# Kernel optimization log

Hardware: AMD Instinct MI355X
Metric: run time of the kernel (lower is better)

Reference implementation:

```python
import jax, jax.numpy as jnp
import numpy as np

N_NODES = 100000
N_EDGES = 1600000
IN_F, HID, N_CLS = 512, 64, 32


def gcn_conv(x, edge_index, W, b, num_nodes):
    """PyG GCNConv: h = D^{-1/2} (A+I) D^{-1/2} (x W) + b."""
    loop = jnp.arange(num_nodes)
    src = jnp.concatenate([edge_index[0], loop])  # [E+N]
    dst = jnp.concatenate([edge_index[1], loop])
    # degree of target nodes (incl. self-loops)
    deg = jax.ops.segment_sum(jnp.ones_like(dst, dtype=x.dtype), dst,
                              num_segments=num_nodes)
    dinv = jnp.where(deg > 0, jax.lax.rsqrt(deg), 0.0)
    norm = dinv[src] * dinv[dst]  # [E+N]
    h = x @ W  # dense transform first (matches PyG: small out dim)
    msgs = h[src] * norm[:, None]  # edge-wise gather + scale
    out = jax.ops.segment_sum(msgs, dst, num_segments=num_nodes)  # scatter-add
    return out + b


def setup_inputs() -> dict:
    key = jax.random.key(0)
    k1, k2, k3, k4, k5, k6 = jax.random.split(key, 6)
    x = jax.random.normal(k1, (N_NODES, IN_F), dtype=jnp.float32)
    edge_index = jax.random.randint(k2, (2, N_EDGES), 0, N_NODES, dtype=jnp.int64)
    # Glorot-style init for the two GCNConv weights + biases
    W1 = jax.random.normal(k3, (IN_F, HID), dtype=jnp.float32) / np.sqrt(IN_F)
    b1 = jnp.zeros((HID,), dtype=jnp.float32)
    W2 = jax.random.normal(k4, (HID, N_CLS), dtype=jnp.float32) / np.sqrt(HID)
    b2 = jnp.zeros((N_CLS,), dtype=jnp.float32)
    return {"x": x, "edge_index": edge_index, "W1": W1, "b1": b1,
            "W2": W2, "b2": b2}


def reference(x, edge_index, W1, b1, W2, b2):
    num_nodes = x.shape[0]
    h = jax.nn.relu(gcn_conv(x, edge_index, W1, b1, num_nodes))
    z = gcn_conv(h, edge_index, W2, b2, num_nodes)
    return (h, z)
```

## Files before the change

### kernel.cpp

```cpp
#include <hip/hip_runtime.h>

#define N_NODES 100000
#define N_EDGES 1600000
#define IN_F 512
#define HID 64
#define N_CLS 32
#define NBKT2 391
#define EBLK 8192
#define NBLKA ((N_EDGES + EBLK - 1) / EBLK)

typedef __attribute__((ext_vector_type(8))) short short8;
typedef __attribute__((ext_vector_type(4))) float f32x4;

__device__ __forceinline__ unsigned short f2bf(float f) {
  unsigned int u = __float_as_uint(f);
  u += 0x7FFFu + ((u >> 16) & 1u);
  return (unsigned short)(u >> 16);
}
__device__ __forceinline__ float bf2f(unsigned int s) {
  return __uint_as_float(s << 16);
}

__global__ __launch_bounds__(256) void coarse_hist_k(const int* __restrict__ ei,
                                                     int* __restrict__ bcnt) {
  __shared__ int lh[NBKT2];
  int tid = threadIdx.x;
  for (int b = tid; b < NBKT2; b += 256) lh[b] = 0;
  __syncthreads();
  int e0 = blockIdx.x * EBLK;
  int e1 = min(e0 + EBLK, N_EDGES);
  for (int e = e0 + tid; e < e1; e += 256)
    atomicAdd(&lh[ei[N_EDGES + e] >> 8], 1);
  __syncthreads();
  for (int b = tid; b < NBKT2; b += 256) {
    int c = lh[b];
    if (c) atomicAdd(&bcnt[b], c);
  }
}

__global__ __launch_bounds__(512) void coarse_scan_k(const int* __restrict__ bcnt,
                                                     int* __restrict__ bbase,
                                                     int* __restrict__ bcur) {
  __shared__ int sc[512];
  int tid = threadIdx.x;
  int v = (tid < NBKT2) ? bcnt[tid] : 0;
  sc[tid] = v;
  __syncthreads();
  for (int off = 1; off < 512; off <<= 1) {
    int t = (tid >= off) ? sc[tid - off] : 0;
    __syncthreads();
    sc[tid] += t;
    __syncthreads();
  }
  int incl = sc[tid];
  int excl = incl - v;
  if (tid < NBKT2) { bbase[tid] = excl; bcur[tid] = excl; }
  if (tid == NBKT2 - 1) bbase[NBKT2] = incl;
}

__global__ __launch_bounds__(256) void passA_k(const int* __restrict__ ei,
                                               int* __restrict__ bcur,
                                               unsigned* __restrict__ tmp) {
  __shared__ int lhist[NBKT2];
  __shared__ int gcur[NBKT2];
  int tid = threadIdx.x;
  int e0 = blockIdx.x * EBLK;
  int e1 = min(e0 + EBLK, N_EDGES);
  for (int b = tid; b < NBKT2; b += 256) lhist[b] = 0;
  __syncthreads();
  for (int e = e0 + tid; e < e1; e += 256) {
    int d = ei[N_EDGES + e];
    atomicAdd(&lhist[d >> 8], 1);
  }
  __syncthreads();
  for (int b = tid; b < NBKT2; b += 256) {
    int c = lhist[b];
    gcur[b] = c ? atomicAdd(&bcur[b], c) : 0;
  }
  __syncthreads();
  for (int e = e0 + tid; e < e1; e += 256) {
    int s = ei[e], d = ei[N_EDGES + e];
    int p = atomicAdd(&gcur[d >> 8], 1);
    tmp[p] = ((unsigned)s << 8) | (unsigned)(d & 255);
  }
}

__global__ __launch_bounds__(256) void passB_k(const unsigned* __restrict__ tmp,
                                               const int* __restrict__ bbase,
                                               int* __restrict__ rowptr,
                                               float* __restrict__ dinv,
                                               int* __restrict__ srcs) {
  __shared__ int sc[256];
  __shared__ int cur[256];
  int b = blockIdx.x, tid = threadIdx.x;
  int n0 = b << 8;
  int n1 = min(n0 + 256, N_NODES);
  int base = bbase[b], end = bbase[b + 1];
  sc[tid] = 0;
  __syncthreads();
  for (int i = base + tid; i < end; i += 256)
    atomicAdd(&sc[tmp[i] & 255u], 1);
  __syncthreads();
  int myc = sc[tid];
  for (int off = 1; off < 256; off <<= 1) {
    int t = (tid >= off) ? sc[tid - off] : 0;
    __syncthreads();
    sc[tid] += t;
    __syncthreads();
  }
  int incl = sc[tid];
  int excl = incl - myc;
  if (n0 + tid < n1) {
    rowptr[n0 + tid + 1] = base + incl;
    dinv[n0 + tid] = rsqrtf((float)(myc + 1));
  }
  if (b == 0 && tid == 0) rowptr[0] = 0;
  cur[tid] = base + excl;
  __syncthreads();
  for (int i = base + tid; i < end; i += 256) {
    unsigned v = tmp[i];
    int p = atomicAdd(&cur[v & 255u], 1);
    srcs[p] = (int)(v >> 8);
  }
}

__global__ __launch_bounds__(256) void w1t_k(const float* __restrict__ W1,
                                             unsigned short* __restrict__ W1t) {
  int i = blockIdx.x * 256 + threadIdx.x;
  if (i < IN_F * HID) {
    int n = i >> 9, k = i & 511;
    W1t[i] = f2bf(W1[(size_t)k * HID + n]);
  }
}

__global__ __launch_bounds__(256) void gemm1_mfma_k(const float* __restrict__ x,
                                                    const unsigned short* __restrict__ W1t,
                                                    const float* __restrict__ dinv,
                                                    unsigned short* __restrict__ h0s) {
  __shared__ __align__(16) char As[64 * 128];
  __shared__ __align__(16) char Ws[64 * 128];
  int tid = threadIdx.x;
  int wave = tid >> 6, lane = tid & 63;
  int row0 = blockIdx.x * 64;
  f32x4 acc[4] = {{0.f,0.f,0.f,0.f},{0.f,0.f,0.f,0.f},{0.f,0.f,0.f,0.f},{0.f,0.f,0.f,0.f}};

  int l15 = lane & 15, lhi = lane >> 4;
  int rA = (wave << 4) + l15;

  for (int k0 = 0; k0 < IN_F; k0 += 64) {
    #pragma unroll
    for (int i = 0; i < 4; ++i) {
      int f = tid + i * 256;
      int r = f >> 4, c4 = (f & 15) << 2;
      float4 v = make_float4(0.f, 0.f, 0.f, 0.f);
      int gr = row0 + r;
      if (gr < N_NODES) v = *(const float4*)(x + (size_t)gr * IN_F + k0 + c4);
      ushort4 u;
      u.x = f2bf(v.x); u.y = f2bf(v.y); u.z = f2bf(v.z); u.w = f2bf(v.w);
      int byte = r * 128 + (c4 << 1);
      byte ^= (r & 7) << 4;
      *(ushort4*)(As + byte) = u;
    }
    #pragma unroll
    for (int i = 0; i < 2; ++i) {
      int f = tid + i * 256;
      int n = f >> 3, k8 = (f & 7) << 3;
      uint4 v = *(const uint4*)(W1t + (size_t)n * IN_F + k0 + k8);
      int byte = n * 128 + (k8 << 1);
      byte ^= (n & 7) << 4;
      *(uint4*)(Ws + byte) = v;
    }
    __syncthreads();
    #pragma unroll
    for (int ks = 0; ks < 64; ks += 32) {
      int kk = ks + (lhi << 3);
      int ba = rA * 128 + (kk << 1); ba ^= (rA & 7) << 4;
      short8 a = *(const short8*)(As + ba);
      #pragma unroll
      for (int j = 0; j < 4; ++j) {
        int nB = (j << 4) + l15;
        int bb = nB * 128 + (kk << 1); bb ^= (nB & 7) << 4;
        short8 bv = *(const short8*)(Ws + bb);
        acc[j] = __builtin_amdgcn_mfma_f32_16x16x32_bf16(a, bv, acc[j], 0, 0, 0);
      }
    }
    __syncthreads();
  }
  int rbase = row0 + (wave << 4) + (lhi << 2);
  #pragma unroll
  for (int r = 0; r < 4; ++r) {
    int gr = rbase + r;
    if (gr < N_NODES) {
      float dn = dinv[gr];
      #pragma unroll
      for (int j = 0; j < 4; ++j)
        h0s[(size_t)gr * HID + (j << 4) + l15] = f2bf(dn * acc[j][r]);
    }
  }
}

__global__ __launch_bounds__(256) void agg1_k(const uint4* __restrict__ h0q,
                                              const int* __restrict__ rowptr,
                                              const int* __restrict__ srcs,
                                              const float* __restrict__ dinv,
                                              const float* __restrict__ b1,
                                              float* __restrict__ out) {
  int idx = blockIdx.x * 256 + threadIdx.x;
  int node = idx >> 6;
  if (node >= N_NODES) return;
  int lane = threadIdx.x & 63;
  int fl = lane & 7, g = lane >> 3;
  int p0 = rowptr[node], p1 = rowptr[node + 1];
  int c = p1 - p0;
  int ps = p0 + ((c * g) >> 3);
  int pe = p0 + ((c * (g + 1)) >> 3);
  float a[8] = {0.f,0.f,0.f,0.f,0.f,0.f,0.f,0.f};
  if (g == 0) {
    uint4 u = h0q[(size_t)node * 8 + fl];
    a[0] = bf2f(u.x & 0xffffu); a[1] = bf2f(u.x >> 16);
    a[2] = bf2f(u.y & 0xffffu); a[3] = bf2f(u.y >> 16);
    a[4] = bf2f(u.z & 0xffffu); a[5] = bf2f(u.z >> 16);
    a[6] = bf2f(u.w & 0xffffu); a[7] = bf2f(u.w >> 16);
  }
  int p = ps;
  for (; p + 2 <= pe; p += 2) {
    int s0 = srcs[p], s1 = srcs[p + 1];
    uint4 u0 = h0q[(size_t)s0 * 8 + fl];
    uint4 u1 = h0q[(size_t)s1 * 8 + fl];
    a[0] += bf2f(u0.x & 0xffffu) + bf2f(u1.x & 0xffffu);
    a[1] += bf2f(u0.x >> 16)     + bf2f(u1.x >> 16);
    a[2] += bf2f(u0.y & 0xffffu) + bf2f(u1.y & 0xffffu);
    a[3] += bf2f(u0.y >> 16)     + bf2f(u1.y >> 16);
    a[4] += bf2f(u0.z & 0xffffu) + bf2f(u1.z & 0xffffu);
    a[5] += bf2f(u0.z >> 16)     + bf2f(u1.z >> 16);
    a[6] += bf2f(u0.w & 0xffffu) + bf2f(u1.w & 0xffffu);
    a[7] += bf2f(u0.w >> 16)     + bf2f(u1.w >> 16);
  }
  if (p < pe) {
    uint4 u = h0q[(size_t)srcs[p] * 8 + fl];
    a[0] += bf2f(u.x & 0xffffu); a[1] += bf2f(u.x >> 16);
    a[2] += bf2f(u.y & 0xffffu); a[3] += bf2f(u.y >> 16);
    a[4] += bf2f(u.z & 0xffffu); a[5] += bf2f(u.z >> 16);
    a[6] += bf2f(u.w & 0xffffu); a[7] += bf2f(u.w >> 16);
  }
  #pragma unroll
  for (int off = 8; off < 64; off <<= 1) {
    #pragma unroll
    for (int i = 0; i < 8; ++i) a[i] += __shfl_xor(a[i], off);
  }
  if (g == 0) {
    float dn = dinv[node];
    float4 bA = *(const float4*)(b1 + fl * 8);
    float4 bB = *(const float4*)(b1 + fl * 8 + 4);
    float4 s0, s1;
    s0.x = fmaxf(dn * a[0] + bA.x, 0.f); s0.y = fmaxf(dn * a[1] + bA.y, 0.f);
    s0.z = fmaxf(dn * a[2] + bA.z, 0.f); s0.w = fmaxf(dn * a[3] + bA.w, 0.f);
    s1.x = fmaxf(dn * a[4] + bB.x, 0.f); s1.y = fmaxf(dn * a[5] + bB.y, 0.f);
    s1.z = fmaxf(dn * a[6] + bB.z, 0.f); s1.w = fmaxf(dn * a[7] + bB.w, 0.f);
    *(float4*)(out + (size_t)node * HID + fl * 8) = s0;
    *(float4*)(out + (size_t)node * HID + fl * 8 + 4) = s1;
  }
}

__global__ __launch_bounds__(256) void gemm2_k(const float* __restrict__ h,
                                               const float* __restrict__ W2,
                                               const float* __restrict__ dinv,
                                               unsigned short* __restrict__ h2b) {
  __shared__ float w2s[HID * N_CLS];
  __shared__ float hs[32][HID];
  int tid = threadIdx.x;
  for (int i = tid; i < HID * N_CLS; i += 256) w2s[i] = W2[i];
  int node0 = blockIdx.x * 32;
  for (int i = tid; i < 32 * HID / 4; i += 256) {
    int r = i >> 4, c4 = (i & 15) << 2;
    int g = node0 + r;
    float4 v = make_float4(0.f, 0.f, 0.f, 0.f);
    if (g < N_NODES) v = *(const float4*)(h + (size_t)g * HID + c4);
    *(float4*)&hs[r][c4] = v;
  }
  __syncthreads();
  int cls = tid & 31, nl = tid >> 5;
  float acc[4] = {0.f, 0.f, 0.f, 0.f};
  #pragma unroll
  for (int k = 0; k < HID; ++k) {
    float w = w2s[k * N_CLS + cls];
    #pragma unroll
    for (int j = 0; j < 4; ++j) acc[j] += hs[nl * 4 + j][k] * w;
  }
  #pragma unroll
  for (int j = 0; j < 4; ++j) {
    int g = node0 + nl * 4 + j;
    if (g < N_NODES) h2b[(size_t)g * N_CLS + cls] = f2bf(dinv[g] * acc[j]);
  }
}

__global__ __launch_bounds__(256) void agg2_k(const uint2* __restrict__ h2u,
                                              const int* __restrict__ rowptr,
                                              const int* __restrict__ srcs,
                                              const float* __restrict__ dinv,
                                              const float* __restrict__ b2,
                                              float* __restrict__ out) {
  int idx = blockIdx.x * 256 + threadIdx.x;
  int node = idx >> 6;
  if (node >= N_NODES) return;
  int lane = threadIdx.x & 63;
  int fl = lane & 7, g = lane >> 3;
  int p0 = rowptr[node], p1 = rowptr[node + 1];
  int c = p1 - p0;
  int ps = p0 + ((c * g) >> 3);
  int pe = p0 + ((c * (g + 1)) >> 3);
  float a0 = 0.f, a1 = 0.f, a2 = 0.f, a3 = 0.f;
  if (g == 0) {
    uint2 u = h2u[(size_t)node * 8 + fl];
    a0 = bf2f(u.x & 0xffffu); a1 = bf2f(u.x >> 16);
    a2 = bf2f(u.y & 0xffffu); a3 = bf2f(u.y >> 16);
  }
  int p = ps;
  for (; p + 2 <= pe; p += 2) {
    int s0 = srcs[p], s1 = srcs[p + 1];
    uint2 u0 = h2u[(size_t)s0 * 8 + fl];
    uint2 u1 = h2u[(size_t)s1 * 8 + fl];
    a0 += bf2f(u0.x & 0xffffu) + bf2f(u1.x & 0xffffu);
    a1 += bf2f(u0.x >> 16)     + bf2f(u1.x >> 16);
    a2 += bf2f(u0.y & 0xffffu) + bf2f(u1.y & 0xffffu);
    a3 += bf2f(u0.y >> 16)     + bf2f(u1.y >> 16);
  }
  if (p < pe) {
    uint2 u = h2u[(size_t)srcs[p] * 8 + fl];
    a0 += bf2f(u.x & 0xffffu); a1 += bf2f(u.x >> 16);
    a2 += bf2f(u.y & 0xffffu); a3 += bf2f(u.y >> 16);
  }
  #pragma unroll
  for (int off = 8; off < 64; off <<= 1) {
    a0 += __shfl_xor(a0, off); a1 += __shfl_xor(a1, off);
    a2 += __shfl_xor(a2, off); a3 += __shfl_xor(a3, off);
  }
  if (g == 0) {
    float dn = dinv[node];
    float4 bv = *(const float4*)(b2 + fl * 4);
    float4 st;
    st.x = dn * a0 + bv.x; st.y = dn * a1 + bv.y;
    st.z = dn * a2 + bv.z; st.w = dn * a3 + bv.w;
    *(float4*)(out + (size_t)node * N_CLS + fl * 4) = st;
  }
}

extern "C" void kernel_launch(void* const* d_in, const int* in_sizes, int n_in,
                              void* d_out, int out_size, void* d_ws, size_t ws_size,
                              hipStream_t stream) {
  const float* x  = (const float*)d_in[0];
  const int*   ei = (const int*)d_in[1];
  const float* W1 = (const float*)d_in[2];
  const float* b1 = (const float*)d_in[3];
  const float* W2 = (const float*)d_in[4];
  const float* b2 = (const float*)d_in[5];
  float* out_h = (float*)d_out;
  float* out_z = out_h + (size_t)N_NODES * HID;

  char* ws = (char*)d_ws;
  int* bcnt           = (int*)(ws + 0);
  int* bbase          = (int*)(ws + (4 << 10));
  int* bcur           = (int*)(ws + (8 << 10));
  int* rowptr         = (int*)(ws + (16 << 10));
  float* dinv         = (float*)(ws + (528 << 10));
  unsigned short* W1t = (unsigned short*)(ws + (944 << 10));
  unsigned* tmp       = (unsigned*)(ws + (1024 << 10));
  int* srcs           = (int*)(ws + (8ull << 20));
  unsigned short* h0s = (unsigned short*)(ws + (15ull << 20));
  unsigned short* h2b = (unsigned short*)(ws + (28ull << 20));

  hipMemsetAsync(bcnt, 0, NBKT2 * sizeof(int), stream);
  w1t_k<<<(IN_F * HID + 255) / 256, 256, 0, stream>>>(W1, W1t);
  coarse_hist_k<<<NBLKA, 256, 0, stream>>>(ei, bcnt);
  coarse_scan_k<<<1, 512, 0, stream>>>(bcnt, bbase, bcur);
  passA_k<<<NBLKA, 256, 0, stream>>>(ei, bcur, tmp);
  passB_k<<<NBKT2, 256, 0, stream>>>(tmp, bbase, rowptr, dinv, srcs);
  gemm1_mfma_k<<<(N_NODES + 63) / 64, 256, 0, stream>>>(x, W1t, dinv, h0s);
  agg1_k<<<(N_NODES * 64) / 256, 256, 0, stream>>>((const uint4*)h0s, rowptr, srcs, dinv, b1, out_h);
  gemm2_k<<<(N_NODES + 31) / 32, 256, 0, stream>>>(out_h, W2, dinv, h2b);
  agg2_k<<<(N_NODES * 64) / 256, 256, 0, stream>>>((const uint2*)h2b, rowptr, srcs, dinv, b2, out_z);
}
```

Measured before the change: 232.8 us.

## Split features into 16-wide slabs and aggregate each slab in separate passes

The GEMM outputs are now written as slab-major arrays of 16 bf16 features per node (3.2 MB per slab), and the aggregation runs once per slab: four passes for layer 1 and two for layer 2. A single generic kernel replaces both aggregation kernels. The aim is a gather working set small enough to stay in L2/MALL, so random neighbour reads hit cache instead of HBM. In exchange the edge list and rowptr are re-read on every pass, more kernels are launched, and each gather fetches only 4 bytes per lane.

```diff
diff --git a/kernel.cpp b/kernel.cpp
--- a/kernel.cpp
+++ b/kernel.cpp
@@ -136,7 +136,7 @@
 __global__ __launch_bounds__(256) void gemm1_mfma_k(const float* __restrict__ x,
                                                     const unsigned short* __restrict__ W1t,
                                                     const float* __restrict__ dinv,
-                                                    unsigned short* __restrict__ h0s) {
+                                                    unsigned short* __restrict__ h0q) {
   __shared__ __align__(16) char As[64 * 128];
   __shared__ __align__(16) char Ws[64 * 128];
   int tid = threadIdx.x;
@@ -194,78 +194,65 @@
       float dn = dinv[gr];
       #pragma unroll
       for (int j = 0; j < 4; ++j)
-        h0s[(size_t)gr * HID + (j << 4) + l15] = f2bf(dn * acc[j][r]);
+        h0q[((size_t)j * N_NODES + gr) * 16 + l15] = f2bf(dn * acc[j][r]);
     }
   }
 }
 
-__global__ __launch_bounds__(256) void agg1_k(const uint4* __restrict__ h0q,
+__global__ __launch_bounds__(256) void aggq_k(const unsigned* __restrict__ hq,
                                               const int* __restrict__ rowptr,
                                               const int* __restrict__ srcs,
                                               const float* __restrict__ dinv,
-                                              const float* __restrict__ b1,
-                                              float* __restrict__ out) {
+                                              const float* __restrict__ bias,
+                                              float* __restrict__ out,
+                                              int ostride, int do_relu) {
   int idx = blockIdx.x * 256 + threadIdx.x;
   int node = idx >> 6;
   if (node >= N_NODES) return;
   int lane = threadIdx.x & 63;
-  int fl = lane & 7, g = lane >> 3;
+  int ln = lane & 7, g = lane >> 3;
   int p0 = rowptr[node], p1 = rowptr[node + 1];
   int c = p1 - p0;
   int ps = p0 + ((c * g) >> 3);
   int pe = p0 + ((c * (g + 1)) >> 3);
-  float a[8] = {0.f,0.f,0.f,0.f,0.f,0.f,0.f,0.f};
+  float a0 = 0.f, a1 = 0.f;
   if (g == 0) {
-    uint4 u = h0q[(size_t)node * 8 + fl];
-    a[0] = bf2f(u.x & 0xffffu); a[1] = bf2f(u.x >> 16);
-    a[2] = bf2f(u.y & 0xffffu); a[3] = bf2f(u.y >> 16);
-    a[4] = bf2f(u.z & 0xffffu); a[5] = bf2f(u.z >> 16);
-    a[6] = bf2f(u.w & 0xffffu); a[7] = bf2f(u.w >> 16);
+    unsigned u = hq[(size_t)node * 8 + ln];
+    a0 = bf2f(u & 0xffffu); a1 = bf2f(u >> 16);
   }
   int p = ps;
-  for (; p + 2 <= pe; p += 2) {
-    int s0 = srcs[p], s1 = srcs[p + 1];
-    uint4 u0 = h0q[(size_t)s0 * 8 + fl];
-    uint4 u1 = h0q[(size_t)s1 * 8 + fl];
-    a[0] += bf2f(u0.x & 0xffffu) + bf2f(u1.x & 0xffffu);
-    a[1] += bf2f(u0.x >> 16)     + bf2f(u1.x >> 16);
-    a[2] += bf2f(u0.y & 0xffffu) + bf2f(u1.y & 0xffffu);
-    a[3] += bf2f(u0.y >> 16)     + bf2f(u1.y >> 16);
-    a[4] += bf2f(u0.z & 0xffffu) + bf2f(u1.z & 0xffffu);
-    a[5] += bf2f(u0.z >> 16)     + bf2f(u1.z >> 16);
-    a[6] += bf2f(u0.w & 0xffffu) + bf2f(u1.w & 0xffffu);
-    a[7] += bf2f(u0.w >> 16)     + bf2f(u1.w >> 16);
-  }
-  if (p < pe) {
-    uint4 u = h0q[(size_t)srcs[p] * 8 + fl];
-    a[0] += bf2f(u.x & 0xffffu); a[1] += bf2f(u.x >> 16);
-    a[2] += bf2f(u.y & 0xffffu); a[3] += bf2f(u.y >> 16);
-    a[4] += bf2f(u.z & 0xffffu); a[5] += bf2f(u.z >> 16);
-    a[6] += bf2f(u.w & 0xffffu); a[7] += bf2f(u.w >> 16);
+  for (; p + 4 <= pe; p += 4) {
+    int s0 = srcs[p], s1 = srcs[p + 1], s2 = srcs[p + 2], s3 = srcs[p + 3];
+    unsigned u0 = hq[(size_t)s0 * 8 + ln];
+    unsigned u1 = hq[(size_t)s1 * 8 + ln];
+    unsigned u2 = hq[(size_t)s2 * 8 + ln];
+    unsigned u3 = hq[(size_t)s3 * 8 + ln];
+    a0 += (bf2f(u0 & 0xffffu) + bf2f(u1 & 0xffffu)) + (bf2f(u2 & 0xffffu) + bf2f(u3 & 0xffffu));
+    a1 += (bf2f(u0 >> 16) + bf2f(u1 >> 16)) + (bf2f(u2 >> 16) + bf2f(u3 >> 16));
+  }
+  for (; p < pe; ++p) {
+    unsigned u = hq[(size_t)srcs[p] * 8 + ln];
+    a0 += bf2f(u & 0xffffu); a1 += bf2f(u >> 16);
   }
   #pragma unroll
   for (int off = 8; off < 64; off <<= 1) {
-    #pragma unroll
-    for (int i = 0; i < 8; ++i) a[i] += __shfl_xor(a[i], off);
+    a0 += __shfl_xor(a0, off);
+    a1 += __shfl_xor(a1, off);
   }
   if (g == 0) {
     float dn = dinv[node];
-    float4 bA = *(const float4*)(b1 + fl * 8);
-    float4 bB = *(const float4*)(b1 + fl * 8 + 4);
-    float4 s0, s1;
-    s0.x = fmaxf(dn * a[0] + bA.x, 0.f); s0.y = fmaxf(dn * a[1] + bA.y, 0.f);
-    s0.z = fmaxf(dn * a[2] + bA.z, 0.f); s0.w = fmaxf(dn * a[3] + bA.w, 0.f);
-    s1.x = fmaxf(dn * a[4] + bB.x, 0.f); s1.y = fmaxf(dn * a[5] + bB.y, 0.f);
-    s1.z = fmaxf(dn * a[6] + bB.z, 0.f); s1.w = fmaxf(dn * a[7] + bB.w, 0.f);
-    *(float4*)(out + (size_t)node * HID + fl * 8) = s0;
-    *(float4*)(out + (size_t)node * HID + fl * 8 + 4) = s1;
+    float2 st;
+    st.x = dn * a0 + bias[ln * 2];
+    st.y = dn * a1 + bias[ln * 2 + 1];
+    if (do_relu) { st.x = fmaxf(st.x, 0.f); st.y = fmaxf(st.y, 0.f); }
+    *(float2*)(out + (size_t)node * ostride + ln * 2) = st;
   }
 }
 
 __global__ __launch_bounds__(256) void gemm2_k(const float* __restrict__ h,
                                                const float* __restrict__ W2,
                                                const float* __restrict__ dinv,
-                                               unsigned short* __restrict__ h2b) {
+                                               unsigned short* __restrict__ h2h) {
   __shared__ float w2s[HID * N_CLS];
   __shared__ float hs[32][HID];
   int tid = threadIdx.x;
@@ -280,6 +267,7 @@
   }
   __syncthreads();
   int cls = tid & 31, nl = tid >> 5;
+  int half = cls >> 4, cl = cls & 15;
   float acc[4] = {0.f, 0.f, 0.f, 0.f};
   #pragma unroll
   for (int k = 0; k < HID; ++k) {
@@ -290,58 +278,7 @@
   #pragma unroll
   for (int j = 0; j < 4; ++j) {
     int g = node0 + nl * 4 + j;
-    if (g < N_NODES) h2b[(size_t)g * N_CLS + cls] = f2bf(dinv[g] * acc[j]);
-  }
-}
-
-__global__ __launch_bounds__(256) void agg2_k(const uint2* __restrict__ h2u,
-                                              const int* __restrict__ rowptr,
-                                              const int* __restrict__ srcs,
-                                              const float* __restrict__ dinv,
-                                              const float* __restrict__ b2,
-                                              float* __restrict__ out) {
-  int idx = blockIdx.x * 256 + threadIdx.x;
-  int node = idx >> 6;
-  if (node >= N_NODES) return;
-  int lane = threadIdx.x & 63;
-  int fl = lane & 7, g = lane >> 3;
-  int p0 = rowptr[node], p1 = rowptr[node + 1];
-  int c = p1 - p0;
-  int ps = p0 + ((c * g) >> 3);
-  int pe = p0 + ((c * (g + 1)) >> 3);
-  float a0 = 0.f, a1 = 0.f, a2 = 0.f, a3 = 0.f;
-  if (g == 0) {
-    uint2 u = h2u[(size_t)node * 8 + fl];
-    a0 = bf2f(u.x & 0xffffu); a1 = bf2f(u.x >> 16);
-    a2 = bf2f(u.y & 0xffffu); a3 = bf2f(u.y >> 16);
-  }
-  int p = ps;
-  for (; p + 2 <= pe; p += 2) {
-    int s0 = srcs[p], s1 = srcs[p + 1];
-    uint2 u0 = h2u[(size_t)s0 * 8 + fl];
-    uint2 u1 = h2u[(size_t)s1 * 8 + fl];
-    a0 += bf2f(u0.x & 0xffffu) + bf2f(u1.x & 0xffffu);
-    a1 += bf2f(u0.x >> 16)     + bf2f(u1.x >> 16);
-    a2 += bf2f(u0.y & 0xffffu) + bf2f(u1.y & 0xffffu);
-    a3 += bf2f(u0.y >> 16)     + bf2f(u1.y >> 16);
-  }
-  if (p < pe) {
-    uint2 u = h2u[(size_t)srcs[p] * 8 + fl];
-    a0 += bf2f(u.x & 0xffffu); a1 += bf2f(u.x >> 16);
-    a2 += bf2f(u.y & 0xffffu); a3 += bf2f(u.y >> 16);
-  }
-  #pragma unroll
-  for (int off = 8; off < 64; off <<= 1) {
-    a0 += __shfl_xor(a0, off); a1 += __shfl_xor(a1, off);
-    a2 += __shfl_xor(a2, off); a3 += __shfl_xor(a3, off);
-  }
-  if (g == 0) {
-    float dn = dinv[node];
-    float4 bv = *(const float4*)(b2 + fl * 4);
-    float4 st;
-    st.x = dn * a0 + bv.x; st.y = dn * a1 + bv.y;
-    st.z = dn * a2 + bv.z; st.w = dn * a3 + bv.w;
-    *(float4*)(out + (size_t)node * N_CLS + fl * 4) = st;
+    if (g < N_NODES) h2h[((size_t)half * N_NODES + g) * 16 + cl] = f2bf(dinv[g] * acc[j]);
   }
 }
 
@@ -366,8 +303,8 @@
   unsigned short* W1t = (unsigned short*)(ws + (944 << 10));
   unsigned* tmp       = (unsigned*)(ws + (1024 << 10));
   int* srcs           = (int*)(ws + (8ull << 20));
-  unsigned short* h0s = (unsigned short*)(ws + (15ull << 20));
-  unsigned short* h2b = (unsigned short*)(ws + (28ull << 20));
+  unsigned short* h0q = (unsigned short*)(ws + (15ull << 20));
+  unsigned short* h2h = (unsigned short*)(ws + (28ull << 20));
 
   hipMemsetAsync(bcnt, 0, NBKT2 * sizeof(int), stream);
   w1t_k<<<(IN_F * HID + 255) / 256, 256, 0, stream>>>(W1, W1t);
@@ -375,8 +312,14 @@
   coarse_scan_k<<<1, 512, 0, stream>>>(bcnt, bbase, bcur);
   passA_k<<<NBLKA, 256, 0, stream>>>(ei, bcur, tmp);
   passB_k<<<NBKT2, 256, 0, stream>>>(tmp, bbase, rowptr, dinv, srcs);
-  gemm1_mfma_k<<<(N_NODES + 63) / 64, 256, 0, stream>>>(x, W1t, dinv, h0s);
-  agg1_k<<<(N_NODES * 64) / 256, 256, 0, stream>>>((const uint4*)h0s, rowptr, srcs, dinv, b1, out_h);
-  gemm2_k<<<(N_NODES + 31) / 32, 256, 0, stream>>>(out_h, W2, dinv, h2b);
-  agg2_k<<<(N_NODES * 64) / 256, 256, 0, stream>>>((const uint2*)h2b, rowptr, srcs, dinv, b2, out_z);
-}
+  gemm1_mfma_k<<<(N_NODES + 63) / 64, 256, 0, stream>>>(x, W1t, dinv, h0q);
+  for (int q = 0; q < 4; ++q)
+    aggq_k<<<(N_NODES * 64) / 256, 256, 0, stream>>>(
+        (const unsigned*)(h0q + (size_t)q * N_NODES * 16), rowptr, srcs, dinv,
+        b1 + q * 16, out_h + q * 16, HID, 1);
+  gemm2_k<<<(N_NODES + 31) / 32, 256, 0, stream>>>(out_h, W2, dinv, h2h);
+  for (int q = 0; q < 2; ++q)
+    aggq_k<<<(N_NODES * 64) / 256, 256, 0, stream>>>(
+        (const unsigned*)(h2h + (size_t)q * N_NODES * 16), rowptr, srcs, dinv,
+        b2 + q * 16, out_z + q * 16, N_CLS, 0);
+}
```

Result: slower. 368.7 us (+58.3%).

## Fuse layer-2 dense transform into agg1 and reuse per-block edge histograms

Applied to the files above, without the earlier changes.

Fuses the second-layer 64x32 matmul into the first aggregation kernel: each wave writes its relu output row to shared memory and immediately computes the scaled bf16 h2 row, removing the gemm2 kernel and its re-read of out_h. coarse_hist now stores per-block bucket counts so passA no longer re-reads destinations and rebuilds its local histogram. The memset is folded into the W1 transpose kernel. In exchange, every agg1 block reloads W2 into shared memory, and the fused kernel adds shared memory and register use, which may lower occupancy.

```diff
diff --git a/kernel.cpp b/kernel.cpp
--- a/kernel.cpp
+++ b/kernel.cpp
@@ -21,8 +21,20 @@
   return __uint_as_float(s << 16);
 }
 
+__global__ __launch_bounds__(256) void w1t_k(const float* __restrict__ W1,
+                                             unsigned short* __restrict__ W1t,
+                                             int* __restrict__ bcnt) {
+  int i = blockIdx.x * 256 + threadIdx.x;
+  if (i < NBKT2) bcnt[i] = 0;
+  if (i < IN_F * HID) {
+    int n = i >> 9, k = i & 511;
+    W1t[i] = f2bf(W1[(size_t)k * HID + n]);
+  }
+}
+
 __global__ __launch_bounds__(256) void coarse_hist_k(const int* __restrict__ ei,
-                                                     int* __restrict__ bcnt) {
+                                                     int* __restrict__ bcnt,
+                                                     int* __restrict__ bhist) {
   __shared__ int lh[NBKT2];
   int tid = threadIdx.x;
   for (int b = tid; b < NBKT2; b += 256) lh[b] = 0;
@@ -34,6 +46,7 @@
   __syncthreads();
   for (int b = tid; b < NBKT2; b += 256) {
     int c = lh[b];
+    bhist[blockIdx.x * NBKT2 + b] = c;
     if (c) atomicAdd(&bcnt[b], c);
   }
 }
@@ -59,22 +72,15 @@
 }
 
 __global__ __launch_bounds__(256) void passA_k(const int* __restrict__ ei,
+                                               const int* __restrict__ bhist,
                                                int* __restrict__ bcur,
                                                unsigned* __restrict__ tmp) {
-  __shared__ int lhist[NBKT2];
   __shared__ int gcur[NBKT2];
   int tid = threadIdx.x;
   int e0 = blockIdx.x * EBLK;
   int e1 = min(e0 + EBLK, N_EDGES);
-  for (int b = tid; b < NBKT2; b += 256) lhist[b] = 0;
-  __syncthreads();
-  for (int e = e0 + tid; e < e1; e += 256) {
-    int d = ei[N_EDGES + e];
-    atomicAdd(&lhist[d >> 8], 1);
-  }
-  __syncthreads();
   for (int b = tid; b < NBKT2; b += 256) {
-    int c = lhist[b];
+    int c = bhist[blockIdx.x * NBKT2 + b];
     gcur[b] = c ? atomicAdd(&bcur[b], c) : 0;
   }
   __syncthreads();
@@ -121,15 +127,6 @@
     unsigned v = tmp[i];
     int p = atomicAdd(&cur[v & 255u], 1);
     srcs[p] = (int)(v >> 8);
-  }
-}
-
-__global__ __launch_bounds__(256) void w1t_k(const float* __restrict__ W1,
-                                             unsigned short* __restrict__ W1t) {
-  int i = blockIdx.x * 256 + threadIdx.x;
-  if (i < IN_F * HID) {
-    int n = i >> 9, k = i & 511;
-    W1t[i] = f2bf(W1[(size_t)k * HID + n]);
   }
 }
 
@@ -199,16 +196,24 @@
   }
 }
 
-__global__ __launch_bounds__(256) void agg1_k(const uint4* __restrict__ h0q,
-                                              const int* __restrict__ rowptr,
-                                              const int* __restrict__ srcs,
-                                              const float* __restrict__ dinv,
-                                              const float* __restrict__ b1,
-                                              float* __restrict__ out) {
-  int idx = blockIdx.x * 256 + threadIdx.x;
+__global__ __launch_bounds__(256) void agg1g2_k(const uint4* __restrict__ h0q,
+                                                const int* __restrict__ rowptr,
+                                                const int* __restrict__ srcs,
+                                                const float* __restrict__ dinv,
+                                                const float* __restrict__ b1,
+                                                const float* __restrict__ W2,
+                                                float* __restrict__ out_h,
+                                                unsigned short* __restrict__ h2b) {
+  __shared__ float w2s[HID * N_CLS];
+  __shared__ float hrow[4][HID];
+  int tid = threadIdx.x;
+  for (int i = tid; i < HID * N_CLS; i += 256) w2s[i] = W2[i];
+  __syncthreads();
+
+  int idx = blockIdx.x * 256 + tid;
   int node = idx >> 6;
-  if (node >= N_NODES) return;
-  int lane = threadIdx.x & 63;
+  int wv = tid >> 6;
+  int lane = tid & 63;
   int fl = lane & 7, g = lane >> 3;
   int p0 = rowptr[node], p1 = rowptr[node + 1];
   int c = p1 - p0;
@@ -248,8 +253,8 @@
     #pragma unroll
     for (int i = 0; i < 8; ++i) a[i] += __shfl_xor(a[i], off);
   }
+  float dn = dinv[node];
   if (g == 0) {
-    float dn = dinv[node];
     float4 bA = *(const float4*)(b1 + fl * 8);
     float4 bB = *(const float4*)(b1 + fl * 8 + 4);
     float4 s0, s1;
@@ -257,41 +262,19 @@
     s0.z = fmaxf(dn * a[2] + bA.z, 0.f); s0.w = fmaxf(dn * a[3] + bA.w, 0.f);
     s1.x = fmaxf(dn * a[4] + bB.x, 0.f); s1.y = fmaxf(dn * a[5] + bB.y, 0.f);
     s1.z = fmaxf(dn * a[6] + bB.z, 0.f); s1.w = fmaxf(dn * a[7] + bB.w, 0.f);
-    *(float4*)(out + (size_t)node * HID + fl * 8) = s0;
-    *(float4*)(out + (size_t)node * HID + fl * 8 + 4) = s1;
-  }
-}
-
-__global__ __launch_bounds__(256) void gemm2_k(const float* __restrict__ h,
-                                               const float* __restrict__ W2,
-                                               const float* __restrict__ dinv,
-                                               unsigned short* __restrict__ h2b) {
-  __shared__ float w2s[HID * N_CLS];
-  __shared__ float hs[32][HID];
-  int tid = threadIdx.x;
-  for (int i = tid; i < HID * N_CLS; i += 256) w2s[i] = W2[i];
-  int node0 = blockIdx.x * 32;
-  for (int i = tid; i < 32 * HID / 4; i += 256) {
-    int r = i >> 4, c4 = (i & 15) << 2;
-    int g = node0 + r;
-    float4 v = make_float4(0.f, 0.f, 0.f, 0.f);
-    if (g < N_NODES) v = *(const float4*)(h + (size_t)g * HID + c4);
-    *(float4*)&hs[r][c4] = v;
-  }
-  __syncthreads();
-  int cls = tid & 31, nl = tid >> 5;
-  float acc[4] = {0.f, 0.f, 0.f, 0.f};
+    *(float4*)(out_h + (size_t)node * HID + fl * 8) = s0;
+    *(float4*)(out_h + (size_t)node * HID + fl * 8 + 4) = s1;
+    *(float4*)&hrow[wv][fl * 8] = s0;
+    *(float4*)&hrow[wv][fl * 8 + 4] = s1;
+  }
+  int cls = lane & 31, kb = (lane >> 5) << 5;
+  float acc2 = 0.f;
   #pragma unroll
-  for (int k = 0; k < HID; ++k) {
-    float w = w2s[k * N_CLS + cls];
-    #pragma unroll
-    for (int j = 0; j < 4; ++j) acc[j] += hs[nl * 4 + j][k] * w;
-  }
-  #pragma unroll
-  for (int j = 0; j < 4; ++j) {
-    int g = node0 + nl * 4 + j;
-    if (g < N_NODES) h2b[(size_t)g * N_CLS + cls] = f2bf(dinv[g] * acc[j]);
-  }
+  for (int k = 0; k < 32; ++k)
+    acc2 += hrow[wv][kb + k] * w2s[(kb + k) * N_CLS + cls];
+  acc2 += __shfl_xor(acc2, 32);
+  if (lane < 32)
+    h2b[(size_t)node * N_CLS + cls] = f2bf(dn * acc2);
 }
 
 __global__ __launch_bounds__(256) void agg2_k(const uint2* __restrict__ h2u,
@@ -361,22 +344,23 @@
   int* bcnt           = (int*)(ws + 0);
   int* bbase          = (int*)(ws + (4 << 10));
   int* bcur           = (int*)(ws + (8 << 10));
-  int* rowptr         = (int*)(ws + (16 << 10));
-  float* dinv         = (float*)(ws + (528 << 10));
-  unsigned short* W1t = (unsigned short*)(ws + (944 << 10));
-  unsigned* tmp       = (unsigned*)(ws + (1024 << 10));
+  int* bhist          = (int*)(ws + (12 << 10));
+  int* rowptr         = (int*)(ws + (336 << 10));
+  float* dinv         = (float*)(ws + (752 << 10));
+  unsigned short* W1t = (unsigned short*)(ws + (1168 << 10));
+  unsigned* tmp       = (unsigned*)(ws + (1280 << 10));
   int* srcs           = (int*)(ws + (8ull << 20));
   unsigned short* h0s = (unsigned short*)(ws + (15ull << 20));
   unsigned short* h2b = (unsigned short*)(ws + (28ull << 20));
 
-  hipMemsetAsync(bcnt, 0, NBKT2 * sizeof(int), stream);
-  w1t_k<<<(IN_F * HID + 255) / 256, 256, 0, stream>>>(W1, W1t);
-  coarse_hist_k<<<NBLKA, 256, 0, stream>>>(ei, bcnt);
+  w1t_k<<<(IN_F * HID + 255) / 256, 256, 0, stream>>>(W1, W1t, bcnt);
+  coarse_hist_k<<<NBLKA, 256, 0, stream>>>(ei, bcnt, bhist);
   coarse_scan_k<<<1, 512, 0, stream>>>(bcnt, bbase, bcur);
-  passA_k<<<NBLKA, 256, 0, stream>>>(ei, bcur, tmp);
+  passA_k<<<NBLKA, 256, 0, stream>>>(ei, bhist, bcur, tmp);
   passB_k<<<NBKT2, 256, 0, stream>>>(tmp, bbase, rowptr, dinv, srcs);
   gemm1_mfma_k<<<(N_NODES + 63) / 64, 256, 0, stream>>>(x, W1t, dinv, h0s);
-  agg1_k<<<(N_NODES * 64) / 256, 256, 0, stream>>>((const uint4*)h0s, rowptr, srcs, dinv, b1, out_h);
-  gemm2_k<<<(N_NODES + 31) / 32, 256, 0, stream>>>(out_h, W2, dinv, h2b);
-  agg2_k<<<(N_NODES * 64) / 256, 256, 0, stream>>>((const uint2*)h2b, rowptr, srcs, dinv, b2, out_z);
-}
+  agg1g2_k<<<(N_NODES * 64) / 256, 256, 0, stream>>>((const uint4*)h0s, rowptr, srcs,
+                                                     dinv, b1, W2, out_h, h2b);
+  agg2_k<<<(N_NODES * 64) / 256, 256, 0, stream>>>((const uint2*)h2b, rowptr, srcs,
+                                                   dinv, b2, out_z);
+}
```

New measurement: 217.2 us. 1.07x faster.
